# Performance work log

Hardware: AMD Instinct MI355X
Metric: run time of the kernel (lower is better)

The kernel has to match this reference:

```python
import jax, jax.numpy as jnp
import numpy as np

B, T1, T2 = 16, 1024, 1024
K1D, K2D, V1D, V2D, A = 512, 512, 256, 256, 128


def setup_inputs() -> dict:
    key = jax.random.key(0)
    ks = jax.random.split(key, 10)
    inp = {
        "k1": jax.random.normal(ks[0], (B, T1, K1D), dtype=jnp.float32),
        "k2": jax.random.normal(ks[1], (B, T2, K2D), dtype=jnp.float32),
        "v1": jax.random.normal(ks[2], (B, T1, V1D), dtype=jnp.float32),
        "v2": jax.random.normal(ks[3], (B, T2, V2D), dtype=jnp.float32),
        # Linear params (torch nn.Linear: y = x @ W.T + b)
        "W1": jax.random.normal(ks[4], (A, K1D), dtype=jnp.float32) / np.sqrt(K1D),
        "b1": jnp.zeros((A,), dtype=jnp.float32),
        "W2": jax.random.normal(ks[5], (A, K2D), dtype=jnp.float32) / np.sqrt(K2D),
        "b2": jnp.zeros((A,), dtype=jnp.float32),
        # valid lengths in [T/2, T-1] so no softmax row is entirely -inf
        "k1_lengths": jax.random.randint(ks[6], (B,), T1 // 2, T1, dtype=jnp.int32),
        "k2_lengths": jax.random.randint(ks[7], (B,), T2 // 2, T2, dtype=jnp.int32),
    }
    return inp


def reference(k1, k2, v1, v2, W1, b1, W2, b2, k1_lengths, k2_lengths):
    # projections
    q1 = jnp.einsum("bti,ai->bta", k1, W1) + b1  # [B,T1,A]
    q2 = jnp.einsum("bti,ai->bta", k2, W2) + b2  # [B,T2,A]
    # co-attention score [B,T1,T2]
    score = jnp.einsum("bia,bja->bij", q1, q2)
    # faithful mask: torch code adds 1 for rows>=l1 and 1 for cols>=l2,
    # then masks where sum == 1  -> XOR of the two pad conditions.
    row_pad = jnp.arange(T1)[None, :, None] >= k1_lengths[:, None, None]  # [B,T1,1]
    col_pad = jnp.arange(T2)[None, None, :] >= k2_lengths[:, None, None]  # [B,1,T2]
    mask = jnp.logical_xor(row_pad, col_pad)
    score = jnp.where(mask, -jnp.inf, score)
    # dual softmaxes
    w1 = jax.nn.softmax(jnp.swapaxes(score, 1, 2), axis=-1)  # [B,T2,T1]
    w2 = jax.nn.softmax(score, axis=-1)                      # [B,T1,T2]
    o1 = jnp.einsum("bji,bid->bjd", w1, v1)  # [B,T2,V1D]
    o2 = jnp.einsum("bij,bjd->bid", w2, v2)  # [B,T1,V2D]
    # note: the torch module additionally slices w1/w2/score per sample to
    # (l2,l1)/(l1,l2) ragged views; with fixed shapes we return the full
    # tensors (the valid region matches; slicing is a zero-copy view in torch).
    return (o1, o2, w1, w2, score)
```

## Files before the change

### kernel.cpp

```cpp
#include <hip/hip_runtime.h>
#include <math.h>

namespace {
constexpr int TT   = 1024;
constexpr int AD   = 128;
constexpr int KDIM = 512;
constexpr int VDIM = 256;
constexpr int NB   = 16;
constexpr size_t T2T = (size_t)TT * TT;
constexpr size_t BT  = (size_t)NB * TT;
}

#define MASK_VAL (-1.0e30f)

typedef __bf16 bf16x8 __attribute__((ext_vector_type(8)));
typedef float  f32x4  __attribute__((ext_vector_type(4)));

__device__ __forceinline__ unsigned short bf16_rne(float x) {
    unsigned int u = __builtin_bit_cast(unsigned int, x);
    u += 0x7fffu + ((u >> 16) & 1u);
    return (unsigned short)(u >> 16);
}
__device__ __forceinline__ float bf16f(unsigned short h) {
    return __builtin_bit_cast(float, ((unsigned int)h) << 16);
}
__device__ __forceinline__ void split2(float x, unsigned short& h, unsigned short& l) {
    h = bf16_rne(x);
    l = bf16_rne(x - bf16f(h));
}

__global__ __launch_bounds__(256) void prep_fused_kernel(
    const float* __restrict__ v1, const float* __restrict__ v2,
    unsigned short* __restrict__ vth, unsigned short* __restrict__ vtl,
    const float* __restrict__ k1, const float* __restrict__ W1, const float* __restrict__ bias1,
    const float* __restrict__ k2, const float* __restrict__ W2, const float* __restrict__ bias2,
    unsigned short* __restrict__ q1h, unsigned short* __restrict__ q1l,
    unsigned short* __restrict__ q2h, unsigned short* __restrict__ q2l)
{
    __shared__ alignas(16) char smem[40960];
    const int tid = threadIdx.x;

    if (blockIdx.x < 1024) {
        const int pid   = blockIdx.x;
        const int which = pid >> 9;
        const int rest  = pid & 511;
        const int b     = rest & 15;
        const int k0    = (rest >> 4) * 32;
        const float* vb = (which ? v1 : v2) + (size_t)b * TT * VDIM;
        float (*ls)[257] = (float(*)[257])smem;

#pragma unroll
        for (int rep = 0; rep < 8; ++rep) {
            int idx = tid + rep * 256;
            int k  = idx >> 6;
            int n4 = (idx & 63) * 4;
            float4 x = *(const float4*)(vb + (size_t)(k0 + k) * VDIM + n4);
            ls[k][n4 + 0] = x.x;
            ls[k][n4 + 1] = x.y;
            ls[k][n4 + 2] = x.z;
            ls[k][n4 + 3] = x.w;
        }
        __syncthreads();

        const size_t pbase = ((size_t)(which * NB + b)) * VDIM * TT;
#pragma unroll
        for (int rep = 0; rep < 4; ++rep) {
            int idx = tid + rep * 256;
            int n  = idx >> 2;
            int sg = (idx & 3) * 8;
            unsigned short h[8], l[8];
#pragma unroll
            for (int j = 0; j < 8; ++j) {
                float x = ls[sg + j][n];
                split2(x, h[j], l[j]);
            }
            uint4 H, L;
            H.x = (unsigned)h[0] | ((unsigned)h[1] << 16);
            H.y = (unsigned)h[2] | ((unsigned)h[3] << 16);
            H.z = (unsigned)h[4] | ((unsigned)h[5] << 16);
            H.w = (unsigned)h[6] | ((unsigned)h[7] << 16);
            L.x = (unsigned)l[0] | ((unsigned)l[1] << 16);
            L.y = (unsigned)l[2] | ((unsigned)l[3] << 16);
            L.z = (unsigned)l[4] | ((unsigned)l[5] << 16);
            L.w = (unsigned)l[6] | ((unsigned)l[7] << 16);
            size_t off = pbase + (size_t)n * TT + k0 + sg;
            *(uint4*)(vth + off) = H;
            *(uint4*)(vtl + off) = L;
        }
        return;
    }

    const int qid  = blockIdx.x - 1024;
    const int proj = qid >> 7;
    const int m0   = (qid & 127) * 128;
    const float* __restrict__ K    = proj ? k2 : k1;
    const float* __restrict__ W    = proj ? W2 : W1;
    const float* __restrict__ bias = proj ? bias2 : bias1;
    unsigned short* __restrict__ qh = proj ? q2h : q1h;
    unsigned short* __restrict__ ql = proj ? q2l : q1l;

    unsigned short* akh = (unsigned short*)smem;
    unsigned short* akl = akh + 128 * 40;
    unsigned short* bwh = akl + 128 * 40;
    unsigned short* bwl = bwh + 128 * 40;

    const int lane = tid & 63;
    const int wv   = tid >> 6;
    const int wm = wv >> 1, wn = wv & 1;
    const int la = lane & 15, kg = lane >> 4;

    f32x4 acc[4][4];
#pragma unroll
    for (int m = 0; m < 4; ++m)
#pragma unroll
        for (int n = 0; n < 4; ++n) acc[m][n] = (f32x4){0.f, 0.f, 0.f, 0.f};

    for (int k0 = 0; k0 < KDIM; k0 += 32) {
#pragma unroll
        for (int rep = 0; rep < 4; ++rep) {
            int idx = tid + rep * 256;
            int row = idx >> 3, c4 = (idx & 7) * 4;
            float4 x = *(const float4*)(K + (size_t)(m0 + row) * KDIM + k0 + c4);
            ushort4 H, L;
            split2(x.x, H.x, L.x);
            split2(x.y, H.y, L.y);
            split2(x.z, H.z, L.z);
            split2(x.w, H.w, L.w);
            *(ushort4*)&akh[row * 40 + c4] = H;
            *(ushort4*)&akl[row * 40 + c4] = L;
        }
#pragma unroll
        for (int rep = 0; rep < 4; ++rep) {
            int idx = tid + rep * 256;
            int row = idx >> 3, c4 = (idx & 7) * 4;
            float4 x = *(const float4*)(W + (size_t)row * KDIM + k0 + c4);
            ushort4 H, L;
            split2(x.x, H.x, L.x);
            split2(x.y, H.y, L.y);
            split2(x.z, H.z, L.z);
            split2(x.w, H.w, L.w);
            *(ushort4*)&bwh[row * 40 + c4] = H;
            *(ushort4*)&bwl[row * 40 + c4] = L;
        }
        __syncthreads();

        bf16x8 ah[4], al[4], bh[4], bl[4];
#pragma unroll
        for (int m = 0; m < 4; ++m) {
            int r = wm * 64 + m * 16 + la;
            ah[m] = *(const bf16x8*)&akh[r * 40 + kg * 8];
            al[m] = *(const bf16x8*)&akl[r * 40 + kg * 8];
        }
#pragma unroll
        for (int n = 0; n < 4; ++n) {
            int c = wn * 64 + n * 16 + la;
            bh[n] = *(const bf16x8*)&bwh[c * 40 + kg * 8];
            bl[n] = *(const bf16x8*)&bwl[c * 40 + kg * 8];
        }
        __builtin_amdgcn_s_setprio(1);
#pragma unroll
        for (int m = 0; m < 4; ++m)
#pragma unroll
            for (int n = 0; n < 4; ++n) {
                acc[m][n] = __builtin_amdgcn_mfma_f32_16x16x32_bf16(ah[m], bh[n], acc[m][n], 0, 0, 0);
                acc[m][n] = __builtin_amdgcn_mfma_f32_16x16x32_bf16(ah[m], bl[n], acc[m][n], 0, 0, 0);
                acc[m][n] = __builtin_amdgcn_mfma_f32_16x16x32_bf16(al[m], bh[n], acc[m][n], 0, 0, 0);
            }
        __builtin_amdgcn_s_setprio(0);
        __syncthreads();
    }

#pragma unroll
    for (int n = 0; n < 4; ++n) {
        int col = wn * 64 + n * 16 + la;
        float bv = bias[col];
#pragma unroll
        for (int m = 0; m < 4; ++m)
#pragma unroll
            for (int r = 0; r < 4; ++r) {
                int row = m0 + wm * 64 + m * 16 + kg * 4 + r;
                unsigned short h, l;
                split2(acc[m][n][r] + bv, h, l);
                qh[(size_t)row * AD + col] = h;
                ql[(size_t)row * AD + col] = l;
            }
    }
}

__global__ __launch_bounds__(256) void score_mfma_stats_kernel(
    const unsigned short* __restrict__ q1h, const unsigned short* __restrict__ q1l,
    const unsigned short* __restrict__ q2h, const unsigned short* __restrict__ q2l,
    const int* __restrict__ len1, const int* __restrict__ len2,
    float* __restrict__ score,
    float* __restrict__ prm, float* __restrict__ prs,
    float* __restrict__ pcm, float* __restrict__ pcs)
{
    const int b  = blockIdx.x;
    const int mt = blockIdx.y >> 3, nt = blockIdx.y & 7;
    const int m0 = mt * 128, n0 = nt * 128;
    const size_t qoff = (size_t)b * TT * AD;

    __shared__ alignas(16) unsigned short ath[128 * 40];
    __shared__ alignas(16) unsigned short atl[128 * 40];
    __shared__ alignas(16) unsigned short bth[128 * 40];
    __shared__ alignas(16) unsigned short btl[128 * 40];
    __shared__ float red_m[2][128];
    __shared__ float red_s[2][128];

    const int tid  = threadIdx.x;
    const int lane = tid & 63;
    const int wv   = tid >> 6;
    const int wm = wv >> 1, wn = wv & 1;
    const int la = lane & 15, kg = lane >> 4;

    f32x4 acc[4][4];
#pragma unroll
    for (int m = 0; m < 4; ++m)
#pragma unroll
        for (int n = 0; n < 4; ++n) acc[m][n] = (f32x4){0.f, 0.f, 0.f, 0.f};

    for (int k0 = 0; k0 < AD; k0 += 32) {
#pragma unroll
        for (int rep = 0; rep < 2; ++rep) {
            int idx = tid + rep * 256;
            int row = idx >> 2, sg = (idx & 3) * 8;
            *(uint4*)&ath[row * 40 + sg] = *(const uint4*)(q1h + qoff + (size_t)(m0 + row) * AD + k0 + sg);
            *(uint4*)&atl[row * 40 + sg] = *(const uint4*)(q1l + qoff + (size_t)(m0 + row) * AD + k0 + sg);
            *(uint4*)&bth[row * 40 + sg] = *(const uint4*)(q2h + qoff + (size_t)(n0 + row) * AD + k0 + sg);
            *(uint4*)&btl[row * 40 + sg] = *(const uint4*)(q2l + qoff + (size_t)(n0 + row) * AD + k0 + sg);
        }
        __syncthreads();

        bf16x8 ah[4], al[4], bh[4], bl[4];
#pragma unroll
        for (int m = 0; m < 4; ++m) {
            int r = wm * 64 + m * 16 + la;
            ah[m] = *(const bf16x8*)&ath[r * 40 + kg * 8];
            al[m] = *(const bf16x8*)&atl[r * 40 + kg * 8];
        }
#pragma unroll
        for (int n = 0; n < 4; ++n) {
            int c = wn * 64 + n * 16 + la;
            bh[n] = *(const bf16x8*)&bth[c * 40 + kg * 8];
            bl[n] = *(const bf16x8*)&btl[c * 40 + kg * 8];
        }
        __builtin_amdgcn_s_setprio(1);
#pragma unroll
        for (int m = 0; m < 4; ++m)
#pragma unroll
            for (int n = 0; n < 4; ++n) {
                acc[m][n] = __builtin_amdgcn_mfma_f32_16x16x32_bf16(ah[m], bh[n], acc[m][n], 0, 0, 0);
                acc[m][n] = __builtin_amdgcn_mfma_f32_16x16x32_bf16(ah[m], bl[n], acc[m][n], 0, 0, 0);
                acc[m][n] = __builtin_amdgcn_mfma_f32_16x16x32_bf16(al[m], bh[n], acc[m][n], 0, 0, 0);
            }
        __builtin_amdgcn_s_setprio(0);
        __syncthreads();
    }

    const int l1v = len1[b];
    const int l2v = len2[b];

#pragma unroll
    for (int m = 0; m < 4; ++m)
#pragma unroll
        for (int r = 0; r < 4; ++r) {
            int row = m0 + wm * 64 + m * 16 + kg * 4 + r;
            bool rp = row >= l1v;
#pragma unroll
            for (int n = 0; n < 4; ++n) {
                int col = n0 + wn * 64 + n * 16 + la;
                bool cp = col >= l2v;
                if (rp != cp) acc[m][n][r] = MASK_VAL;
            }
        }
    float* sb = score + (size_t)b * T2T;
#pragma unroll
    for (int m = 0; m < 4; ++m)
#pragma unroll
        for (int r = 0; r < 4; ++r) {
            int row = m0 + wm * 64 + m * 16 + kg * 4 + r;
#pragma unroll
            for (int n = 0; n < 4; ++n) {
                int col = n0 + wn * 64 + n * 16 + la;
                sb[(size_t)row * TT + col] = acc[m][n][r];
            }
        }

#pragma unroll
    for (int m = 0; m < 4; ++m)
#pragma unroll
        for (int r = 0; r < 4; ++r) {
            float mr = fmaxf(fmaxf(acc[m][0][r], acc[m][1][r]),
                             fmaxf(acc[m][2][r], acc[m][3][r]));
#pragma unroll
            for (int off = 1; off <= 8; off <<= 1) mr = fmaxf(mr, __shfl_xor(mr, off));
            float sr = __expf(acc[m][0][r] - mr) + __expf(acc[m][1][r] - mr) +
                       __expf(acc[m][2][r] - mr) + __expf(acc[m][3][r] - mr);
#pragma unroll
            for (int off = 1; off <= 8; off <<= 1) sr += __shfl_xor(sr, off);
            if (la == 0) {
                int rloc = wm * 64 + m * 16 + kg * 4 + r;
                red_m[wn][rloc] = mr;
                red_s[wn][rloc] = sr;
            }
        }
    __syncthreads();
    if (tid < 128) {
        float ma = red_m[0][tid], mb2 = red_m[1][tid];
        float mm = fmaxf(ma, mb2);
        float ss = red_s[0][tid] * __expf(ma - mm) + red_s[1][tid] * __expf(mb2 - mm);
        prm[(size_t)nt * BT + (size_t)b * TT + m0 + tid] = mm;
        prs[(size_t)nt * BT + (size_t)b * TT + m0 + tid] = ss;
    }
    __syncthreads();

#pragma unroll
    for (int n = 0; n < 4; ++n) {
        float mc = MASK_VAL;
#pragma unroll
        for (int m = 0; m < 4; ++m)
#pragma unroll
            for (int r = 0; r < 4; ++r) mc = fmaxf(mc, acc[m][n][r]);
#pragma unroll
        for (int off = 16; off <= 32; off <<= 1) mc = fmaxf(mc, __shfl_xor(mc, off));
        float sc = 0.f;
#pragma unroll
        for (int m = 0; m < 4; ++m)
#pragma unroll
            for (int r = 0; r < 4; ++r) sc += __expf(acc[m][n][r] - mc);
#pragma unroll
        for (int off = 16; off <= 32; off <<= 1) sc += __shfl_xor(sc, off);
        if (kg == 0) {
            int cloc = wn * 64 + n * 16 + la;
            red_m[wm][cloc] = mc;
            red_s[wm][cloc] = sc;
        }
    }
    __syncthreads();
    if (tid < 128) {
        float ma = red_m[0][tid], mb2 = red_m[1][tid];
        float mm = fmaxf(ma, mb2);
        float ss = red_s[0][tid] * __expf(ma - mm) + red_s[1][tid] * __expf(mb2 - mm);
        pcm[(size_t)mt * BT + (size_t)b * TT + n0 + tid] = mm;
        pcs[(size_t)mt * BT + (size_t)b * TT + n0 + tid] = ss;
    }
}

__global__ __launch_bounds__(512) void ogemm_fused_kernel(
    const float* __restrict__ score,
    const float* __restrict__ prm, const float* __restrict__ prs,
    const float* __restrict__ pcm, const float* __restrict__ pcs,
    const unsigned short* __restrict__ vth, const unsigned short* __restrict__ vtl,
    float* __restrict__ w2, float* __restrict__ w1,
    float* __restrict__ o2, float* __restrict__ o1)
{
    const int b     = blockIdx.x;
    const int m0    = blockIdx.y * 128;
    const int which = blockIdx.z;
    const size_t vbase = ((size_t)(which * NB + b)) * VDIM * TT;

    const float* __restrict__ sb = score + (size_t)b * T2T;
    float* __restrict__ wout = (which ? w1 : w2) + (size_t)b * T2T;
    float* __restrict__ ob   = (which ? o1 : o2) + (size_t)b * TT * VDIM;

    __shared__ alignas(16) unsigned short awh[2][128 * 40];
    __shared__ alignas(16) unsigned short awl[2][128 * 40];
    __shared__ alignas(16) unsigned short bvh[2][256 * 40];
    __shared__ alignas(16) unsigned short bvl[2][256 * 40];
    __shared__ float st[128][33];
    __shared__ float sm_s[128], si_s[128];

    const int tid  = threadIdx.x;
    const int lane = tid & 63;
    const int wv   = tid >> 6;
    const int wm   = wv >> 2;
    const int wn   = wv & 3;
    const int la = lane & 15, kg = lane >> 4;

    const int r_row0 = tid >> 3,          r_c4_0 = (tid & 7) * 4;
    const int r_row1 = (tid + 512) >> 3,  r_c4_1 = ((tid + 512) & 7) * 4;
    const int c_ip0 = tid >> 5,           c_c4_0 = (tid & 31) * 4;
    const int c_ip1 = (tid + 512) >> 5,   c_c4_1 = ((tid + 512) & 31) * 4;
    const int b_n0 = tid >> 2,            b_sg = (tid & 3) * 8;
    const int b_n1 = b_n0 + 128;

    if (tid < 128) {
        const float* pm = which ? pcm : prm;
        const float* ps = which ? pcs : prs;
        size_t base = (size_t)b * TT + m0 + tid;
        float nm = MASK_VAL;
#pragma unroll
        for (int c = 0; c < 8; ++c) nm = fmaxf(nm, pm[(size_t)c * BT + base]);
        float s = 0.f;
#pragma unroll
        for (int c = 0; c < 8; ++c)
            s += ps[(size_t)c * BT + base] * __expf(pm[(size_t)c * BT + base] - nm);
        sm_s[tid] = nm;
        si_s[tid] = 1.f / s;
    }
    __syncthreads();

    f32x4 acc[4][4];
#pragma unroll
    for (int m = 0; m < 4; ++m)
#pragma unroll
        for (int n = 0; n < 4; ++n) acc[m][n] = (f32x4){0.f, 0.f, 0.f, 0.f};

    float4 aA0, aA1;
    uint4  bh0, bh1, bl0, bl1;

    auto issueA = [&](int k0) {
        if (which == 0) {
            aA0 = *(const float4*)(sb + (size_t)(m0 + r_row0) * TT + k0 + r_c4_0);
            aA1 = *(const float4*)(sb + (size_t)(m0 + r_row1) * TT + k0 + r_c4_1);
        } else {
            aA0 = *(const float4*)(sb + (size_t)(k0 + c_ip0) * TT + m0 + c_c4_0);
            aA1 = *(const float4*)(sb + (size_t)(k0 + c_ip1) * TT + m0 + c_c4_1);
        }
    };
    auto issueB = [&](int k0) {
        size_t off0 = vbase + (size_t)b_n0 * TT + k0 + b_sg;
        size_t off1 = vbase + (size_t)b_n1 * TT + k0 + b_sg;
        bh0 = *(const uint4*)(vth + off0);
        bh1 = *(const uint4*)(vth + off1);
        bl0 = *(const uint4*)(vtl + off0);
        bl1 = *(const uint4*)(vtl + off1);
    };

    issueA(0);
    issueB(0);

    int cur = 0;
    for (int k0 = 0; k0 < TT; k0 += 32, cur ^= 1) {
        unsigned short* AWH = &awh[cur][0];
        unsigned short* AWL = &awl[cur][0];
        unsigned short* BVH = &bvh[cur][0];
        unsigned short* BVL = &bvl[cur][0];

        *(uint4*)&BVH[b_n0 * 40 + b_sg] = bh0;
        *(uint4*)&BVH[b_n1 * 40 + b_sg] = bh1;
        *(uint4*)&BVL[b_n0 * 40 + b_sg] = bl0;
        *(uint4*)&BVL[b_n1 * 40 + b_sg] = bl1;
        if (k0 + 32 < TT) issueB(k0 + 32);

        if (which == 0) {
#pragma unroll
            for (int rep = 0; rep < 2; ++rep) {
                float4 x = rep ? aA1 : aA0;
                int row = rep ? r_row1 : r_row0;
                int c4  = rep ? r_c4_1 : r_c4_0;
                float mm = sm_s[row], ii = si_s[row];
                f32x4 wv4;
                wv4[0] = __expf(x.x - mm) * ii;
                wv4[1] = __expf(x.y - mm) * ii;
                wv4[2] = __expf(x.z - mm) * ii;
                wv4[3] = __expf(x.w - mm) * ii;
                __builtin_nontemporal_store(wv4, (f32x4*)(wout + (size_t)(m0 + row) * TT + k0 + c4));
                ushort4 H, L;
                split2(wv4[0], H.x, L.x);
                split2(wv4[1], H.y, L.y);
                split2(wv4[2], H.z, L.z);
                split2(wv4[3], H.w, L.w);
                *(ushort4*)&AWH[row * 40 + c4] = H;
                *(ushort4*)&AWL[row * 40 + c4] = L;
            }
            if (k0 + 32 < TT) issueA(k0 + 32);
            __syncthreads();
        } else {
            {
                float4 x = aA0;
                st[c_c4_0 + 0][c_ip0] = __expf(x.x - sm_s[c_c4_0 + 0]) * si_s[c_c4_0 + 0];
                st[c_c4_0 + 1][c_ip0] = __expf(x.y - sm_s[c_c4_0 + 1]) * si_s[c_c4_0 + 1];
                st[c_c4_0 + 2][c_ip0] = __expf(x.z - sm_s[c_c4_0 + 2]) * si_s[c_c4_0 + 2];
                st[c_c4_0 + 3][c_ip0] = __expf(x.w - sm_s[c_c4_0 + 3]) * si_s[c_c4_0 + 3];
                x = aA1;
                st[c_c4_1 + 0][c_ip1] = __expf(x.x - sm_s[c_c4_1 + 0]) * si_s[c_c4_1 + 0];
                st[c_c4_1 + 1][c_ip1] = __expf(x.y - sm_s[c_c4_1 + 1]) * si_s[c_c4_1 + 1];
                st[c_c4_1 + 2][c_ip1] = __expf(x.z - sm_s[c_c4_1 + 2]) * si_s[c_c4_1 + 2];
                st[c_c4_1 + 3][c_ip1] = __expf(x.w - sm_s[c_c4_1 + 3]) * si_s[c_c4_1 + 3];
            }
            if (k0 + 32 < TT) issueA(k0 + 32);
            __syncthreads();
#pragma unroll
            for (int rep = 0; rep < 2; ++rep) {
                int idx = tid + rep * 512;
                int j = idx >> 3, i4 = (idx & 7) * 4;
                f32x4 wv4;
                wv4[0] = st[j][i4 + 0];
                wv4[1] = st[j][i4 + 1];
                wv4[2] = st[j][i4 + 2];
                wv4[3] = st[j][i4 + 3];
                __builtin_nontemporal_store(wv4, (f32x4*)(wout + (size_t)(m0 + j) * TT + k0 + i4));
                ushort4 H, L;
                split2(wv4[0], H.x, L.x);
                split2(wv4[1], H.y, L.y);
                split2(wv4[2], H.z, L.z);
                split2(wv4[3], H.w, L.w);
                *(ushort4*)&AWH[j * 40 + i4] = H;
                *(ushort4*)&AWL[j * 40 + i4] = L;
            }
            __syncthreads();
        }

        bf16x8 ah[4], al[4], bh[4], bl[4];
#pragma unroll
        for (int m = 0; m < 4; ++m) {
            int r = wm * 64 + m * 16 + la;
            ah[m] = *(const bf16x8*)&AWH[r * 40 + kg * 8];
            al[m] = *(const bf16x8*)&AWL[r * 40 + kg * 8];
        }
#pragma unroll
        for (int n = 0; n < 4; ++n) {
            int c = wn * 64 + n * 16 + la;
            bh[n] = *(const bf16x8*)&BVH[c * 40 + kg * 8];
            bl[n] = *(const bf16x8*)&BVL[c * 40 + kg * 8];
        }
        __builtin_amdgcn_s_setprio(1);
#pragma unroll
        for (int m = 0; m < 4; ++m)
#pragma unroll
            for (int n = 0; n < 4; ++n) {
                acc[m][n] = __builtin_amdgcn_mfma_f32_16x16x32_bf16(ah[m], bh[n], acc[m][n], 0, 0, 0);
                acc[m][n] = __builtin_amdgcn_mfma_f32_16x16x32_bf16(ah[m], bl[n], acc[m][n], 0, 0, 0);
                acc[m][n] = __builtin_amdgcn_mfma_f32_16x16x32_bf16(al[m], bh[n], acc[m][n], 0, 0, 0);
            }
        __builtin_amdgcn_s_setprio(0);
    }

#pragma unroll
    for (int m = 0; m < 4; ++m)
#pragma unroll
        for (int r = 0; r < 4; ++r) {
            int row = m0 + wm * 64 + m * 16 + kg * 4 + r;
#pragma unroll
            for (int n = 0; n < 4; ++n) {
                int col = wn * 64 + n * 16 + la;
                __builtin_nontemporal_store(acc[m][n][r], ob + (size_t)row * VDIM + col);
            }
        }
}

extern "C" void kernel_launch(void* const* d_in, const int* in_sizes, int n_in,
                              void* d_out, int out_size, void* d_ws, size_t ws_size,
                              hipStream_t stream) {
    const float* k1 = (const float*)d_in[0];
    const float* k2 = (const float*)d_in[1];
    const float* v1 = (const float*)d_in[2];
    const float* v2 = (const float*)d_in[3];
    const float* W1 = (const float*)d_in[4];
    const float* b1 = (const float*)d_in[5];
    const float* W2 = (const float*)d_in[6];
    const float* b2 = (const float*)d_in[7];
    const int* len1 = (const int*)d_in[8];
    const int* len2 = (const int*)d_in[9];

    float* out = (float*)d_out;
    float* o1    = out;
    float* o2    = out + (size_t)NB * TT * VDIM;
    float* w1    = out + (size_t)2 * NB * TT * VDIM;
    float* w2    = w1 + (size_t)NB * T2T;
    float* score = w2 + (size_t)NB * T2T;

    float* ws   = (float*)d_ws;
    float* prm  = ws;
    float* prs  = prm + 8 * BT;
    float* pcm  = prs + 8 * BT;
    float* pcs  = pcm + 8 * BT;
    unsigned short* q1h = (unsigned short*)(pcs + 8 * BT);
    unsigned short* q1l = q1h + BT * AD;
    unsigned short* q2h = q1l + BT * AD;
    unsigned short* q2l = q2h + BT * AD;
    unsigned short* vth = q2l + BT * AD;
    unsigned short* vtl = vth + (size_t)32 * VDIM * TT;

    prep_fused_kernel<<<dim3(1280), 256, 0, stream>>>(v1, v2, vth, vtl,
                                                      k1, W1, b1, k2, W2, b2,
                                                      q1h, q1l, q2h, q2l);
    score_mfma_stats_kernel<<<dim3(NB, 64), 256, 0, stream>>>(q1h, q1l, q2h, q2l,
                                                              len1, len2, score,
                                                              prm, prs, pcm, pcs);
    ogemm_fused_kernel<<<dim3(NB, TT / 128, 2), 512, 0, stream>>>(score, prm, prs, pcm, pcs,
                                                                  vth, vtl, w2, w1, o2, o1);
}
```

Before: 161.4 us.

## Store Q and V operands in MFMA fragment-tiled layout and load directly from global

The prep kernel now writes the bf16 hi/lo splits of Q1/Q2 and transposed V into a layout blocked by 16-row by 32-k tiles, in the exact per-lane fragment order the 16x16x32 MFMA expects. The score and output kernels then load each operand fragment as a single 16-byte global load straight into registers, dropping the LDS staging buffers, their writes, and the barriers around them. This cuts LDS traffic and synchronisation and frees shared memory, which may raise occupancy. The cost is that global load latency is no longer hidden by the explicit register prefetch for the V operand, and the Q projection epilogue now does scattered 2-byte stores into the tiled layout.

```diff
diff --git a/kernel.cpp b/kernel.cpp
--- a/kernel.cpp
+++ b/kernel.cpp
@@ -13,6 +13,7 @@
 
 #define MASK_VAL (-1.0e30f)
 
+
 typedef __bf16 bf16x8 __attribute__((ext_vector_type(8)));
 typedef float  f32x4  __attribute__((ext_vector_type(4)));
 
@@ -27,6 +28,9 @@
 __device__ __forceinline__ void split2(float x, unsigned short& h, unsigned short& l) {
     h = bf16_rne(x);
     l = bf16_rne(x - bf16f(h));
+}
+__device__ __forceinline__ bf16x8 as_bf16x8(uint4 u) {
+    return __builtin_bit_cast(bf16x8, u);
 }
 
 __global__ __launch_bounds__(256) void prep_fused_kernel(
@@ -63,6 +67,7 @@
         __syncthreads();
 
         const size_t pbase = ((size_t)(which * NB + b)) * VDIM * TT;
+        const int kb = k0 >> 5;
 #pragma unroll
         for (int rep = 0; rep < 4; ++rep) {
             int idx = tid + rep * 256;
@@ -83,7 +88,8 @@
             L.y = (unsigned)l[2] | ((unsigned)l[3] << 16);
             L.z = (unsigned)l[4] | ((unsigned)l[5] << 16);
             L.w = (unsigned)l[6] | ((unsigned)l[7] << 16);
-            size_t off = pbase + (size_t)n * TT + k0 + sg;
+            size_t off = pbase + (size_t)(((n >> 4) * 32 + kb) * 512)
+                               + (size_t)(((sg >> 3) * 16 + (n & 15)) * 8);
             *(uint4*)(vth + off) = H;
             *(uint4*)(vtl + off) = L;
         }
@@ -174,16 +180,23 @@
     for (int n = 0; n < 4; ++n) {
         int col = wn * 64 + n * 16 + la;
         float bv = bias[col];
-#pragma unroll
-        for (int m = 0; m < 4; ++m)
+        int kb  = col >> 5;
+        int kgs = (col >> 3) & 3;
+        int e   = col & 7;
+#pragma unroll
+        for (int m = 0; m < 4; ++m) {
+            int rb = (m0 >> 4) + wm * 4 + m;
+            size_t blk = (size_t)(rb * 4 + kb) * 512;
 #pragma unroll
             for (int r = 0; r < 4; ++r) {
-                int row = m0 + wm * 64 + m * 16 + kg * 4 + r;
+                int las = kg * 4 + r;
+                size_t off = blk + (size_t)(kgs * 16 + las) * 8 + e;
                 unsigned short h, l;
                 split2(acc[m][n][r] + bv, h, l);
-                qh[(size_t)row * AD + col] = h;
-                ql[(size_t)row * AD + col] = l;
-            }
+                qh[off] = h;
+                ql[off] = l;
+            }
+        }
     }
 }
 
@@ -200,10 +213,6 @@
     const int m0 = mt * 128, n0 = nt * 128;
     const size_t qoff = (size_t)b * TT * AD;
 
-    __shared__ alignas(16) unsigned short ath[128 * 40];
-    __shared__ alignas(16) unsigned short atl[128 * 40];
-    __shared__ alignas(16) unsigned short bth[128 * 40];
-    __shared__ alignas(16) unsigned short btl[128 * 40];
     __shared__ float red_m[2][128];
     __shared__ float red_s[2][128];
 
@@ -212,6 +221,7 @@
     const int wv   = tid >> 6;
     const int wm = wv >> 1, wn = wv & 1;
     const int la = lane & 15, kg = lane >> 4;
+    const int slot8 = (kg * 16 + la) * 8;
 
     f32x4 acc[4][4];
 #pragma unroll
@@ -219,30 +229,22 @@
 #pragma unroll
         for (int n = 0; n < 4; ++n) acc[m][n] = (f32x4){0.f, 0.f, 0.f, 0.f};
 
-    for (int k0 = 0; k0 < AD; k0 += 32) {
-#pragma unroll
-        for (int rep = 0; rep < 2; ++rep) {
-            int idx = tid + rep * 256;
-            int row = idx >> 2, sg = (idx & 3) * 8;
-            *(uint4*)&ath[row * 40 + sg] = *(const uint4*)(q1h + qoff + (size_t)(m0 + row) * AD + k0 + sg);
-            *(uint4*)&atl[row * 40 + sg] = *(const uint4*)(q1l + qoff + (size_t)(m0 + row) * AD + k0 + sg);
-            *(uint4*)&bth[row * 40 + sg] = *(const uint4*)(q2h + qoff + (size_t)(n0 + row) * AD + k0 + sg);
-            *(uint4*)&btl[row * 40 + sg] = *(const uint4*)(q2l + qoff + (size_t)(n0 + row) * AD + k0 + sg);
-        }
-        __syncthreads();
-
+#pragma unroll
+    for (int kb = 0; kb < 4; ++kb) {
         bf16x8 ah[4], al[4], bh[4], bl[4];
 #pragma unroll
         for (int m = 0; m < 4; ++m) {
-            int r = wm * 64 + m * 16 + la;
-            ah[m] = *(const bf16x8*)&ath[r * 40 + kg * 8];
-            al[m] = *(const bf16x8*)&atl[r * 40 + kg * 8];
+            int rb = (m0 >> 4) + wm * 4 + m;
+            size_t off = qoff + (size_t)((rb * 4 + kb) * 512) + slot8;
+            ah[m] = as_bf16x8(*(const uint4*)(q1h + off));
+            al[m] = as_bf16x8(*(const uint4*)(q1l + off));
         }
 #pragma unroll
         for (int n = 0; n < 4; ++n) {
-            int c = wn * 64 + n * 16 + la;
-            bh[n] = *(const bf16x8*)&bth[c * 40 + kg * 8];
-            bl[n] = *(const bf16x8*)&btl[c * 40 + kg * 8];
+            int rb = (n0 >> 4) + wn * 4 + n;
+            size_t off = qoff + (size_t)((rb * 4 + kb) * 512) + slot8;
+            bh[n] = as_bf16x8(*(const uint4*)(q2h + off));
+            bl[n] = as_bf16x8(*(const uint4*)(q2l + off));
         }
         __builtin_amdgcn_s_setprio(1);
 #pragma unroll
@@ -254,7 +256,6 @@
                 acc[m][n] = __builtin_amdgcn_mfma_f32_16x16x32_bf16(al[m], bh[n], acc[m][n], 0, 0, 0);
             }
         __builtin_amdgcn_s_setprio(0);
-        __syncthreads();
     }
 
     const int l1v = len1[b];
@@ -365,8 +366,6 @@
 
     __shared__ alignas(16) unsigned short awh[2][128 * 40];
     __shared__ alignas(16) unsigned short awl[2][128 * 40];
-    __shared__ alignas(16) unsigned short bvh[2][256 * 40];
-    __shared__ alignas(16) unsigned short bvl[2][256 * 40];
     __shared__ float st[128][33];
     __shared__ float sm_s[128], si_s[128];
 
@@ -376,13 +375,12 @@
     const int wm   = wv >> 2;
     const int wn   = wv & 3;
     const int la = lane & 15, kg = lane >> 4;
+    const int slot8 = (kg * 16 + la) * 8;
 
     const int r_row0 = tid >> 3,          r_c4_0 = (tid & 7) * 4;
     const int r_row1 = (tid + 512) >> 3,  r_c4_1 = ((tid + 512) & 7) * 4;
     const int c_ip0 = tid >> 5,           c_c4_0 = (tid & 31) * 4;
     const int c_ip1 = (tid + 512) >> 5,   c_c4_1 = ((tid + 512) & 31) * 4;
-    const int b_n0 = tid >> 2,            b_sg = (tid & 3) * 8;
-    const int b_n1 = b_n0 + 128;
 
     if (tid < 128) {
         const float* pm = which ? pcm : prm;
@@ -407,8 +405,6 @@
         for (int n = 0; n < 4; ++n) acc[m][n] = (f32x4){0.f, 0.f, 0.f, 0.f};
 
     float4 aA0, aA1;
-    uint4  bh0, bh1, bl0, bl1;
-
     auto issueA = [&](int k0) {
         if (which == 0) {
             aA0 = *(const float4*)(sb + (size_t)(m0 + r_row0) * TT + k0 + r_c4_0);
@@ -418,30 +414,14 @@
             aA1 = *(const float4*)(sb + (size_t)(k0 + c_ip1) * TT + m0 + c_c4_1);
         }
     };
-    auto issueB = [&](int k0) {
-        size_t off0 = vbase + (size_t)b_n0 * TT + k0 + b_sg;
-        size_t off1 = vbase + (size_t)b_n1 * TT + k0 + b_sg;
-        bh0 = *(const uint4*)(vth + off0);
-        bh1 = *(const uint4*)(vth + off1);
-        bl0 = *(const uint4*)(vtl + off0);
-        bl1 = *(const uint4*)(vtl + off1);
-    };
 
     issueA(0);
-    issueB(0);
 
     int cur = 0;
     for (int k0 = 0; k0 < TT; k0 += 32, cur ^= 1) {
         unsigned short* AWH = &awh[cur][0];
         unsigned short* AWL = &awl[cur][0];
-        unsigned short* BVH = &bvh[cur][0];
-        unsigned short* BVL = &bvl[cur][0];
-
-        *(uint4*)&BVH[b_n0 * 40 + b_sg] = bh0;
-        *(uint4*)&BVH[b_n1 * 40 + b_sg] = bh1;
-        *(uint4*)&BVL[b_n0 * 40 + b_sg] = bl0;
-        *(uint4*)&BVL[b_n1 * 40 + b_sg] = bl1;
-        if (k0 + 32 < TT) issueB(k0 + 32);
+        const int kb = k0 >> 5;
 
         if (which == 0) {
 #pragma unroll
@@ -504,16 +484,16 @@
 
         bf16x8 ah[4], al[4], bh[4], bl[4];
 #pragma unroll
+        for (int n = 0; n < 4; ++n) {
+            size_t off = vbase + (size_t)(((wn * 4 + n) * 32 + kb) * 512) + slot8;
+            bh[n] = as_bf16x8(*(const uint4*)(vth + off));
+            bl[n] = as_bf16x8(*(const uint4*)(vtl + off));
+        }
+#pragma unroll
         for (int m = 0; m < 4; ++m) {
             int r = wm * 64 + m * 16 + la;
             ah[m] = *(const bf16x8*)&AWH[r * 40 + kg * 8];
             al[m] = *(const bf16x8*)&AWL[r * 40 + kg * 8];
-        }
-#pragma unroll
-        for (int n = 0; n < 4; ++n) {
-            int c = wn * 64 + n * 16 + la;
-            bh[n] = *(const bf16x8*)&BVH[c * 40 + kg * 8];
-            bl[n] = *(const bf16x8*)&BVL[c * 40 + kg * 8];
         }
         __builtin_amdgcn_s_setprio(1);
 #pragma unroll
```

After: 162.2 us. Within noise of the previous version (+0.5%).
